# Kernel tuning notes

Hardware: AMD Instinct MI355X
Metric: run time of the kernel (lower is better)

## Reference

```python
import math
import jax, jax.numpy as jnp
import numpy as np

B, T = 65536, 34
VOCAB, TOK_DIM, POS_DIM, D_MODEL, FFN_DIM, HEAD_DIM = 14, 2, 3, 5, 2, 5
EPS = 1e-5

def _pos_flat_idx():
    # replicate _build_pos_map: 10 digits, Z_HI, 10 digits, Z_HI, 10 digits, special0, special1
    sources, indices = [], []
    for _ in range(3):
        for i in range(10):
            sources.append(0); indices.append(i)
        sources.append(2); indices.append(len([s for s in sources if s == 2]) - 1)
    # fix: the torch code appends (2,0),(2,1) after first two digit blocks and (1,0),(2,2) after the third
    sources, indices = [], []
    for i in range(10): sources.append(0); indices.append(i)
    sources.append(2); indices.append(0)
    for i in range(10): sources.append(0); indices.append(i)
    sources.append(2); indices.append(1)
    for i in range(10): sources.append(0); indices.append(i)
    sources.append(1); indices.append(0)
    sources.append(2); indices.append(2)
    src = np.array(sources); idx = np.array(indices)
    # table layout: rows 0..9 digit_pos, row 10 z_hi_pos, rows 11..13 special (learned0, learned1, eos)
    offs = np.array([0, 10, 11])
    return offs[src] + idx  # (34,)

POS_FLAT = jnp.asarray(_pos_flat_idx())
CAUSAL = jnp.tril(jnp.ones((T, T), dtype=bool))

def _rms(x, w):
    return x * jax.lax.rsqrt(jnp.mean(x * x, -1, keepdims=True) + EPS) * w

def setup_inputs():
    key = jax.random.key(0)
    ks = jax.random.split(key, 16)
    n = lambda i, shape: jax.random.normal(ks[i], shape, jnp.float32) * 0.5
    return {
        'idx': jax.random.randint(ks[0], (B, T), 0, VOCAB),
        'tok_emb': n(1, (VOCAB, TOK_DIM)),
        'spiral_amp': jnp.float32(1.0),
        'spiral_phase': jnp.float32(0.1),
        'spiral_slope': jnp.float32(1.0 / 9.0),
        'spiral_offset': jnp.float32(0.05),
        'pos_corr_slope': jnp.float32(0.01),
        'pos_corr_intercept': jnp.float32(0.02),
        'z_hi_pos': n(2, (1, POS_DIM)),
        'special_pos': n(3, (2, POS_DIM)),
        'q_w': n(4, (HEAD_DIM, POS_DIM)),
        'v_w': n(5, (HEAD_DIM, TOK_DIM)),
        'out_A': n(6, (HEAD_DIM, 2)),
        'out_B': n(7, (2, D_MODEL)),
        'q_phase': n(8, (1,)),
        'ln1_w': jnp.ones((D_MODEL,), jnp.float32),
        'ln2_w': jnp.ones((D_MODEL,), jnp.float32),
        'lnf_w': jnp.ones((D_MODEL,), jnp.float32),
        'fc1_w': n(9, (FFN_DIM, D_MODEL)),
        'fc1_b': n(10, (FFN_DIM,)),
        'fc2_w': n(11, (D_MODEL, FFN_DIM)),
        'fc2_b': n(12, (D_MODEL,)),
        'head_w': n(13, (TOK_DIM, D_MODEL)),
    }

def reference(idx, tok_emb, spiral_amp, spiral_phase, spiral_slope, spiral_offset,
              pos_corr_slope, pos_corr_intercept, z_hi_pos, special_pos,
              q_w, v_w, out_A, out_B, q_phase, ln1_w, ln2_w, lnf_w,
              fc1_w, fc1_b, fc2_w, fc2_b, head_w):
    # learned spiral digit positions (10, 3)
    i = jnp.arange(10, dtype=jnp.float32)
    angle = 2.0 * math.pi * i / 10.0 + spiral_phase
    base = jnp.stack([spiral_amp * jnp.cos(angle),
                      spiral_amp * jnp.sin(angle),
                      spiral_slope * i + spiral_offset], -1)
    corr = pos_corr_intercept + pos_corr_slope * i
    digit_pos = base * (1.0 + corr)[:, None]
    table = jnp.concatenate([digit_pos, z_hi_pos, special_pos,
                             jnp.zeros((1, POS_DIM), jnp.float32)], 0)  # (14, 3)
    pos = table[POS_FLAT]  # (T, 3)

    tok = tok_emb[idx]  # (B, T, 2)
    x = jnp.concatenate([tok, jnp.broadcast_to(pos, (idx.shape[0], T, POS_DIM))], -1)  # (B,T,5)

    h = _rms(x, ln1_w)
    q = jnp.einsum('btp,dp->btd', h[..., TOK_DIM:], q_w)  # (B,T,5)
    k = q  # q_proj applied to same input for both q and k
    v = jnp.einsum('btp,dp->btd', h[..., :TOK_DIM], v_w)  # (B,T,5)

    # per-head 2D rotation on first 4 dims (HEAD_DIM//2 = 2 pairs), dim 4 unchanged
    c, s = jnp.cos(q_phase[0]), jnp.sin(q_phase[0])
    q0, q1 = q[..., 0:4:2], q[..., 1:4:2]
    q_rot = jnp.concatenate([
        jnp.stack([q0 * c - q1 * s, q0 * s + q1 * c], -1).reshape(q.shape[:-1] + (4,)),
        q[..., 4:]], -1)

    att = jnp.einsum('btd,bsd->bts', q_rot, k) / math.sqrt(HEAD_DIM)
    att = jnp.where(CAUSAL, att, -jnp.inf)
    att = jax.nn.softmax(att, -1)
    out = jnp.einsum('bts,bsd->btd', att, v)  # (B,T,5)

    x = x + (out @ out_A) @ out_B  # low-rank out_proj
    hh = _rms(x, ln2_w)
    x = x + (jax.nn.gelu(hh @ fc1_w.T + fc1_b, approximate=False) @ fc2_w.T + fc2_b)
    x = _rms(x, lnf_w)
    return (x @ head_w.T) @ tok_emb.T  # (B, T, 14)
```

## Files before the change

kernel.cpp:

```cpp
#include <hip/hip_runtime.h>
#include <math.h>

#define T_SEQ 34
#define NTOK 14
#define NE (T_SEQ * NTOK)
#define ROWS 30
#define BLK 512
#define NEL (ROWS * T_SEQ)
#define AVS (ROWS + 1)
#define TTS (ROWS + 1)

__global__ __launch_bounds__(BLK, 4) void micro_fused_kernel(
    const int* __restrict__ idx,
    const float* __restrict__ tok_emb,
    const float* __restrict__ s_amp, const float* __restrict__ s_phase,
    const float* __restrict__ s_slope, const float* __restrict__ s_offset,
    const float* __restrict__ pc_slope, const float* __restrict__ pc_int,
    const float* __restrict__ z_hi, const float* __restrict__ spec,
    const float* __restrict__ q_w, const float* __restrict__ v_w,
    const float* __restrict__ out_A, const float* __restrict__ out_B,
    const float* __restrict__ q_phase,
    const float* __restrict__ ln1_w, const float* __restrict__ ln2_w,
    const float* __restrict__ lnf_w,
    const float* __restrict__ fc1_w, const float* __restrict__ fc1_b,
    const float* __restrict__ fc2_w, const float* __restrict__ fc2_b,
    const float* __restrict__ head_w,
    float* __restrict__ out, int N)
{
    __shared__ float4 H4[NE];
    __shared__ float  H1f[NE];
    __shared__ float4 C3[NE];
    __shared__ float2 Av[T_SEQ * AVS];
    __shared__ int    toksT[T_SEQ * TTS];
    alignas(16) __shared__ float PosT[T_SEQ * 3];
    alignas(16) __shared__ float TE[NTOK * 2];
    alignas(16) __shared__ float PMs[12];
    alignas(16) __shared__ float WsT[NTOK * 8];
    alignas(16) __shared__ float ln2s[8], lnfs[8], fc1ws[12], fc2ws[12], fc2bs[8];
    __shared__ float fc1bs[2];

    const int tid = threadIdx.x;
    const int b0 = blockIdx.x * ROWS;
    const int elemBase = b0 * T_SEQ;

    for (int i = tid; i < NEL; i += BLK) {
        int g = elemBase + i;
        int v = (g < N) ? idx[g] : 0;
        int r = i / T_SEQ, s = i - r * T_SEQ;
        toksT[s * TTS + r] = v;
    }

    if (tid < NE) {
        const float amp = s_amp[0], ph = s_phase[0], slp = s_slope[0], off = s_offset[0];
        const float pcs = pc_slope[0], pci = pc_int[0];
        const float cph = cosf(q_phase[0]), sph = sinf(q_phase[0]);
        const float cscale = 0.44721359549995793f * 1.4426950408889634f;
        const int e = tid;
        const int t = e / NTOK, tk = e - t * NTOK;
        float px, py, pz;
        if (t == 33)      { px = 0.f;     py = 0.f;     pz = 0.f; }
        else if (t == 32) { px = z_hi[0]; py = z_hi[1]; pz = z_hi[2]; }
        else if (t == 10) { px = spec[0]; py = spec[1]; pz = spec[2]; }
        else if (t == 21) { px = spec[3]; py = spec[4]; pz = spec[5]; }
        else {
            int i = (t < 10) ? t : (t < 21 ? t - 11 : t - 22);
            float fi = (float)i;
            float ang = 0.62831853071795864769f * fi + ph;
            float mlt = 1.f + pci + pcs * fi;
            px = amp * cosf(ang) * mlt;
            py = amp * sinf(ang) * mlt;
            pz = (slp * fi + off) * mlt;
        }
        if (tk == 0) { PosT[t*3] = px; PosT[t*3+1] = py; PosT[t*3+2] = pz; }
        float x0 = tok_emb[tk * 2], x1 = tok_emb[tk * 2 + 1];
        float ssum = x0*x0 + x1*x1 + px*px + py*py + pz*pz;
        float rn = rsqrtf(ssum * 0.2f + 1e-5f);
        float h0 = x0 * rn * ln1_w[0], h1 = x1 * rn * ln1_w[1];
        float h2 = px * rn * ln1_w[2], h3 = py * rn * ln1_w[3], h4 = pz * rn * ln1_w[4];
        float q0 = q_w[0]  * h2 + q_w[1]  * h3 + q_w[2]  * h4;
        float q1 = q_w[3]  * h2 + q_w[4]  * h3 + q_w[5]  * h4;
        float q2 = q_w[6]  * h2 + q_w[7]  * h3 + q_w[8]  * h4;
        float q3 = q_w[9]  * h2 + q_w[10] * h3 + q_w[11] * h4;
        float q4 = q_w[12] * h2 + q_w[13] * h3 + q_w[14] * h4;
        float r0 = q0 * cph - q1 * sph, r1 = q0 * sph + q1 * cph;
        float r2c = q2 * cph - q3 * sph, r3 = q2 * sph + q3 * cph;
        float c0 = (r0*q_w[0] + r1*q_w[3] + r2c*q_w[6] + r3*q_w[9]  + q4*q_w[12]) * cscale;
        float c1 = (r0*q_w[1] + r1*q_w[4] + r2c*q_w[7] + r3*q_w[10] + q4*q_w[13]) * cscale;
        float c2 = (r0*q_w[2] + r1*q_w[5] + r2c*q_w[8] + r3*q_w[11] + q4*q_w[14]) * cscale;
        H4[e] = make_float4(h2, h3, h4, h0);
        H1f[e] = h1;
        C3[e] = make_float4(c0, c1, c2, 0.f);
    }
    if (tid < 28) TE[tid] = tok_emb[tid];
    if (tid < 70) {
        int v = tid / 5, d = tid - v * 5;
        WsT[v * 8 + d] = head_w[d] * tok_emb[v * 2] + head_w[5 + d] * tok_emb[v * 2 + 1];
    }
    if (tid < 10) {
        int j = tid >> 1, c = tid & 1;
        float acc = 0.f;
        for (int i = 0; i < 5; ++i) {
            float m5 = out_A[i*2] * out_B[j] + out_A[i*2+1] * out_B[5 + j];
            acc += m5 * v_w[i*2 + c];
        }
        PMs[tid] = acc;
    }
    if (tid < 5)  { ln2s[tid] = ln2_w[tid]; lnfs[tid] = lnf_w[tid]; fc2bs[tid] = fc2_b[tid]; }
    if (tid < 10) { fc1ws[tid] = fc1_w[tid]; fc2ws[tid] = fc2_w[tid]; }
    if (tid < 2)  { fc1bs[tid] = fc1_b[tid]; }

    __syncthreads();

    auto attn = [&](int t, int rr) {
        int tokt = toksT[t * TTS + rr];
        float4 c3 = C3[t * NTOK + tokt];
        float l = 0.f, a0 = 0.f, a1 = 0.f;
#pragma unroll 2
        for (int s = 0; s <= t; ++s) {
            int tok = toksT[s * TTS + rr];
            int e = s * NTOK + tok;
            float4 h = H4[e];
            float h1v = H1f[e];
            float sc = fmaf(c3.x, h.x, fmaf(c3.y, h.y, c3.z * h.z));
            float p = exp2f(sc);
            l += p;
            a0 = fmaf(p, h.w, a0);
            a1 = fmaf(p, h1v, a1);
        }
        float il = 1.f / l;
        Av[t * AVS + rr] = make_float2(a0 * il, a1 * il);
    };

    if (tid < 17 * ROWS) {
        int p = tid / ROWS;
        int r = tid - p * ROWS;
        attn(p, r);
        attn(33 - p, r);
    }

    __syncthreads();

    float zA[5], zB[5];
    int linA = elemBase + tid;
    int linB = elemBase + tid + BLK;
    bool va = (linA < N);
    bool vb = (tid + BLK < NEL) && (linB < N);

    auto prep = [&](int e2, float* z) {
        int rr = e2 / T_SEQ;
        int t = e2 - rr * T_SEQ;
        int tok = toksT[t * TTS + rr];
        float2 a = Av[t * AVS + rr];
        float xv0 = TE[tok * 2], xv1 = TE[tok * 2 + 1];
        float xv2 = PosT[t*3], xv3 = PosT[t*3+1], xv4 = PosT[t*3+2];

        float y[5];
#pragma unroll
        for (int j = 0; j < 5; ++j)
            y[j] = (j == 0 ? xv0 : j == 1 ? xv1 : j == 2 ? xv2 : j == 3 ? xv3 : xv4)
                 + PMs[j*2] * a.x + PMs[j*2+1] * a.y;

        float s2 = y[0]*y[0] + y[1]*y[1] + y[2]*y[2] + y[3]*y[3] + y[4]*y[4];
        float r2 = rsqrtf(s2 * 0.2f + 1e-5f);
        float hh[5];
#pragma unroll
        for (int j = 0; j < 5; ++j) hh[j] = y[j] * r2 * ln2s[j];

        float u0 = fc1bs[0], u1 = fc1bs[1];
#pragma unroll
        for (int j = 0; j < 5; ++j) { u0 += hh[j] * fc1ws[j]; u1 += hh[j] * fc1ws[5 + j]; }
        float g0 = 0.5f * u0 * (1.f + erff(u0 * 0.70710678118654752f));
        float g1v = 0.5f * u1 * (1.f + erff(u1 * 0.70710678118654752f));

        float y2[5]; float s3 = 0.f;
#pragma unroll
        for (int j = 0; j < 5; ++j) {
            y2[j] = y[j] + g0 * fc2ws[j * 2] + g1v * fc2ws[j * 2 + 1] + fc2bs[j];
            s3 += y2[j] * y2[j];
        }
        float r3 = rsqrtf(s3 * 0.2f + 1e-5f);
#pragma unroll
        for (int j = 0; j < 5; ++j) z[j] = y2[j] * r3 * lnfs[j];
    };

    if (va) prep(tid, zA);
    if (vb) prep(tid + BLK, zB);

    float2* opA = (float2*)(out + (size_t)linA * 14);
    float2* opB = (float2*)(out + (size_t)linB * 14);
#pragma unroll
    for (int v = 0; v < 7; ++v) {
        float4 w0 = *(const float4*)&WsT[(2*v) * 8];
        float  w4 = WsT[(2*v) * 8 + 4];
        float4 u0 = *(const float4*)&WsT[(2*v+1) * 8];
        float  u4 = WsT[(2*v+1) * 8 + 4];
        if (va) {
            float rA = zA[0]*w0.x + zA[1]*w0.y + zA[2]*w0.z + zA[3]*w0.w + zA[4]*w4;
            float rB = zA[0]*u0.x + zA[1]*u0.y + zA[2]*u0.z + zA[3]*u0.w + zA[4]*u4;
            opA[v] = make_float2(rA, rB);
        }
        if (vb) {
            float rA = zB[0]*w0.x + zB[1]*w0.y + zB[2]*w0.z + zB[3]*w0.w + zB[4]*w4;
            float rB = zB[0]*u0.x + zB[1]*u0.y + zB[2]*u0.z + zB[3]*u0.w + zB[4]*u4;
            opB[v] = make_float2(rA, rB);
        }
    }
}

extern "C" void kernel_launch(void* const* d_in, const int* in_sizes, int n_in,
                              void* d_out, int out_size, void* d_ws, size_t ws_size,
                              hipStream_t stream) {
    const int N = in_sizes[0];
    const int grid = (N + NEL - 1) / NEL;
    micro_fused_kernel<<<grid, BLK, 0, stream>>>(
        (const int*)d_in[0],
        (const float*)d_in[1], (const float*)d_in[2], (const float*)d_in[3],
        (const float*)d_in[4], (const float*)d_in[5], (const float*)d_in[6],
        (const float*)d_in[7], (const float*)d_in[8], (const float*)d_in[9],
        (const float*)d_in[10], (const float*)d_in[11], (const float*)d_in[12],
        (const float*)d_in[13], (const float*)d_in[14], (const float*)d_in[15],
        (const float*)d_in[16], (const float*)d_in[17], (const float*)d_in[18],
        (const float*)d_in[19], (const float*)d_in[20], (const float*)d_in[21],
        (const float*)d_in[22],
        (float*)d_out, N);
}
```

Measured before the change: 237.1 us.

## Factor key vectors into per-position weights times per-element norm and fuse paired attention rows

Attention scores are rewritten as a dot of the query coefficients with a per-position weighted position vector, scaled by the per-element RMS factor. This removes the per-element H4/H1f tables in favour of a smaller PW array plus an Rt table. The two rows each thread handles are merged into one loop that shares token and key loads over the common prefix, and fast exp2/rcp intrinsics are used. The launch-bounds occupancy hint is also dropped. This cuts LDS traffic and loop overhead, but it shifts register and occupancy behaviour and lowers the precision of the reciprocal.

```diff
diff --git a/kernel.cpp b/kernel.cpp
--- a/kernel.cpp
+++ b/kernel.cpp
@@ -10,7 +10,7 @@
 #define AVS (ROWS + 1)
 #define TTS (ROWS + 1)
 
-__global__ __launch_bounds__(BLK, 4) void micro_fused_kernel(
+__global__ __launch_bounds__(BLK) void micro_fused_kernel(
     const int* __restrict__ idx,
     const float* __restrict__ tok_emb,
     const float* __restrict__ s_amp, const float* __restrict__ s_phase,
@@ -27,9 +27,9 @@
     const float* __restrict__ head_w,
     float* __restrict__ out, int N)
 {
-    __shared__ float4 H4[NE];
-    __shared__ float  H1f[NE];
     __shared__ float4 C3[NE];
+    __shared__ float4 Rt[NE];
+    __shared__ float4 PW[T_SEQ];
     __shared__ float2 Av[T_SEQ * AVS];
     __shared__ int    toksT[T_SEQ * TTS];
     alignas(16) __shared__ float PosT[T_SEQ * 3];
@@ -71,7 +71,10 @@
             py = amp * sinf(ang) * mlt;
             pz = (slp * fi + off) * mlt;
         }
-        if (tk == 0) { PosT[t*3] = px; PosT[t*3+1] = py; PosT[t*3+2] = pz; }
+        if (tk == 0) {
+            PosT[t*3] = px; PosT[t*3+1] = py; PosT[t*3+2] = pz;
+            PW[t] = make_float4(px * ln1_w[2], py * ln1_w[3], pz * ln1_w[4], 0.f);
+        }
         float x0 = tok_emb[tk * 2], x1 = tok_emb[tk * 2 + 1];
         float ssum = x0*x0 + x1*x1 + px*px + py*py + pz*pz;
         float rn = rsqrtf(ssum * 0.2f + 1e-5f);
@@ -87,9 +90,8 @@
         float c0 = (r0*q_w[0] + r1*q_w[3] + r2c*q_w[6] + r3*q_w[9]  + q4*q_w[12]) * cscale;
         float c1 = (r0*q_w[1] + r1*q_w[4] + r2c*q_w[7] + r3*q_w[10] + q4*q_w[13]) * cscale;
         float c2 = (r0*q_w[2] + r1*q_w[5] + r2c*q_w[8] + r3*q_w[11] + q4*q_w[14]) * cscale;
-        H4[e] = make_float4(h2, h3, h4, h0);
-        H1f[e] = h1;
         C3[e] = make_float4(c0, c1, c2, 0.f);
+        Rt[e] = make_float4(rn, h0, h1, 0.f);
     }
     if (tid < 28) TE[tid] = tok_emb[tid];
     if (tid < 70) {
@@ -111,31 +113,43 @@
 
     __syncthreads();
 
-    auto attn = [&](int t, int rr) {
-        int tokt = toksT[t * TTS + rr];
-        float4 c3 = C3[t * NTOK + tokt];
-        float l = 0.f, a0 = 0.f, a1 = 0.f;
-#pragma unroll 2
-        for (int s = 0; s <= t; ++s) {
-            int tok = toksT[s * TTS + rr];
-            int e = s * NTOK + tok;
-            float4 h = H4[e];
-            float h1v = H1f[e];
-            float sc = fmaf(c3.x, h.x, fmaf(c3.y, h.y, c3.z * h.z));
-            float p = exp2f(sc);
-            l += p;
-            a0 = fmaf(p, h.w, a0);
-            a1 = fmaf(p, h1v, a1);
-        }
-        float il = 1.f / l;
-        Av[t * AVS + rr] = make_float2(a0 * il, a1 * il);
-    };
-
     if (tid < 17 * ROWS) {
         int p = tid / ROWS;
-        int r = tid - p * ROWS;
-        attn(p, r);
-        attn(33 - p, r);
+        int rr = tid - p * ROWS;
+        int t1 = p, t2 = 33 - p;
+        const int* tRow = &toksT[rr];
+        int tok1 = tRow[t1 * TTS];
+        int tok2 = tRow[t2 * TTS];
+        float4 c31 = C3[t1 * NTOK + tok1];
+        float4 c32 = C3[t2 * NTOK + tok2];
+        float l1 = 0.f, a10 = 0.f, a11 = 0.f;
+        float l2 = 0.f, a20 = 0.f, a21 = 0.f;
+
+#pragma unroll 2
+        for (int s = 0; s <= p; ++s) {
+            int tok = tRow[s * TTS];
+            float4 R = Rt[s * NTOK + tok];
+            float4 pw = PW[s];
+            float d1 = fmaf(c31.x, pw.x, fmaf(c31.y, pw.y, c31.z * pw.z));
+            float d2 = fmaf(c32.x, pw.x, fmaf(c32.y, pw.y, c32.z * pw.z));
+            float p1 = __builtin_amdgcn_exp2f(d1 * R.x);
+            float p2 = __builtin_amdgcn_exp2f(d2 * R.x);
+            l1 += p1; a10 = fmaf(p1, R.y, a10); a11 = fmaf(p1, R.z, a11);
+            l2 += p2; a20 = fmaf(p2, R.y, a20); a21 = fmaf(p2, R.z, a21);
+        }
+#pragma unroll 4
+        for (int s = p + 1; s <= t2; ++s) {
+            int tok = tRow[s * TTS];
+            float4 R = Rt[s * NTOK + tok];
+            float4 pw = PW[s];
+            float d2 = fmaf(c32.x, pw.x, fmaf(c32.y, pw.y, c32.z * pw.z));
+            float p2 = __builtin_amdgcn_exp2f(d2 * R.x);
+            l2 += p2; a20 = fmaf(p2, R.y, a20); a21 = fmaf(p2, R.z, a21);
+        }
+        float il1 = __builtin_amdgcn_rcpf(l1);
+        float il2 = __builtin_amdgcn_rcpf(l2);
+        Av[t1 * AVS + rr] = make_float2(a10 * il1, a11 * il1);
+        Av[t2 * AVS + rr] = make_float2(a20 * il2, a21 * il2);
     }
 
     __syncthreads();
```

Result: slower. 242.8 us (+2.4%).

## Precompute factored attention score tables in a setup kernel and slim main kernel

Applied to the files above, without the earlier changes.

A small setup kernel now builds tables in workspace: per-(query position, token) rows of pre-multiplied score coefficients against every key position's scaled positional vector, plus per-(position, token) norm factors and the small weight tables. The main kernel then computes each attention score as a single multiply of a table entry by the key's norm factor, then exp2, reading score rows from global/L2 in float4 chunks. This removes the per-block recomputation of the positional tables and most of the score FMAs. The main kernel also moves to 256-thread blocks with 15 rows and uses the hardware exp2/rcp intrinsics. The cost is an extra kernel launch per call and global-memory reads of the score table. The original fused kernel is kept as a fallback when the workspace is too small.

```diff
diff --git a/kernel.cpp b/kernel.cpp
--- a/kernel.cpp
+++ b/kernel.cpp
@@ -4,13 +4,272 @@
 #define T_SEQ 34
 #define NTOK 14
 #define NE (T_SEQ * NTOK)
-#define ROWS 30
-#define BLK 512
+
+#define OFF_RT   0
+#define OFF_POS  476
+#define OFF_MISC 510
+#define NF4_SHARED 566
+#define OFF_DTAB 566
+#define DROW_F 36
+#define NF4_TOTAL (NF4_SHARED + NE * (DROW_F/4))
+#define WS_NEED ((size_t)NF4_TOTAL * 16)
+#define MI_TE    0
+#define MI_WST   32
+#define MI_PM    144
+#define MI_LN2   160
+#define MI_LNF   168
+#define MI_FC1W  176
+#define MI_FC1B  186
+#define MI_FC2W  192
+#define MI_FC2B  208
+
+#define ROWS 15
+#define BLK 256
 #define NEL (ROWS * T_SEQ)
-#define AVS (ROWS + 1)
-#define TTS (ROWS + 1)
-
-__global__ __launch_bounds__(BLK, 4) void micro_fused_kernel(
+#define TTS 17
+#define AVS 17
+
+__device__ inline void pos_for_t(int t,
+    float amp, float ph, float slp, float off, float pcs, float pci,
+    const float* __restrict__ z_hi, const float* __restrict__ spec,
+    float& px, float& py, float& pz)
+{
+    if (t == 33)      { px = 0.f;     py = 0.f;     pz = 0.f; }
+    else if (t == 32) { px = z_hi[0]; py = z_hi[1]; pz = z_hi[2]; }
+    else if (t == 10) { px = spec[0]; py = spec[1]; pz = spec[2]; }
+    else if (t == 21) { px = spec[3]; py = spec[4]; pz = spec[5]; }
+    else {
+        int i = (t < 10) ? t : (t < 21 ? t - 11 : t - 22);
+        float fi = (float)i;
+        float ang = 0.62831853071795864769f * fi + ph;
+        float mlt = 1.f + pci + pcs * fi;
+        px = amp * cosf(ang) * mlt;
+        py = amp * sinf(ang) * mlt;
+        pz = (slp * fi + off) * mlt;
+    }
+}
+
+__global__ __launch_bounds__(64) void setup_kernel(
+    const float* __restrict__ tok_emb,
+    const float* __restrict__ s_amp, const float* __restrict__ s_phase,
+    const float* __restrict__ s_slope, const float* __restrict__ s_offset,
+    const float* __restrict__ pc_slope, const float* __restrict__ pc_int,
+    const float* __restrict__ z_hi, const float* __restrict__ spec,
+    const float* __restrict__ q_w, const float* __restrict__ v_w,
+    const float* __restrict__ out_A, const float* __restrict__ out_B,
+    const float* __restrict__ q_phase,
+    const float* __restrict__ ln1_w, const float* __restrict__ ln2_w,
+    const float* __restrict__ lnf_w,
+    const float* __restrict__ fc1_w, const float* __restrict__ fc1_b,
+    const float* __restrict__ fc2_w, const float* __restrict__ fc2_b,
+    const float* __restrict__ head_w,
+    float4* __restrict__ ws)
+{
+    __shared__ float4 PWs[T_SEQ];
+    __shared__ float4 Poss[T_SEQ];
+
+    const int tid = threadIdx.x;
+    const float amp = s_amp[0], ph = s_phase[0], slp = s_slope[0], off = s_offset[0];
+    const float pcs = pc_slope[0], pci = pc_int[0];
+
+    if (tid < T_SEQ) {
+        float px, py, pz;
+        pos_for_t(tid, amp, ph, slp, off, pcs, pci, z_hi, spec, px, py, pz);
+        PWs[tid]  = make_float4(px * ln1_w[2], py * ln1_w[3], pz * ln1_w[4], 0.f);
+        Poss[tid] = make_float4(px, py, pz, 0.f);
+    }
+    __syncthreads();
+
+    const int q = blockIdx.x * 64 + tid;
+    if (q < NE) {
+        const int t = q / NTOK, tk = q - t * NTOK;
+        const float cph = cosf(q_phase[0]), sph = sinf(q_phase[0]);
+        const float cscale = 0.44721359549995793f * 1.4426950408889634f;
+        float4 P = Poss[t];
+        float px = P.x, py = P.y, pz = P.z;
+        float x0 = tok_emb[tk * 2], x1 = tok_emb[tk * 2 + 1];
+        float ssum = x0*x0 + x1*x1 + px*px + py*py + pz*pz;
+        float rn = rsqrtf(ssum * 0.2f + 1e-5f);
+        float h0 = x0 * rn * ln1_w[0], h1 = x1 * rn * ln1_w[1];
+        float h2 = px * rn * ln1_w[2], h3 = py * rn * ln1_w[3], h4 = pz * rn * ln1_w[4];
+        float q0 = q_w[0]  * h2 + q_w[1]  * h3 + q_w[2]  * h4;
+        float q1 = q_w[3]  * h2 + q_w[4]  * h3 + q_w[5]  * h4;
+        float q2 = q_w[6]  * h2 + q_w[7]  * h3 + q_w[8]  * h4;
+        float q3 = q_w[9]  * h2 + q_w[10] * h3 + q_w[11] * h4;
+        float q4 = q_w[12] * h2 + q_w[13] * h3 + q_w[14] * h4;
+        float r0 = q0 * cph - q1 * sph, r1 = q0 * sph + q1 * cph;
+        float r2c = q2 * cph - q3 * sph, r3 = q2 * sph + q3 * cph;
+        float c0 = (r0*q_w[0] + r1*q_w[3] + r2c*q_w[6] + r3*q_w[9]  + q4*q_w[12]) * cscale;
+        float c1 = (r0*q_w[1] + r1*q_w[4] + r2c*q_w[7] + r3*q_w[10] + q4*q_w[13]) * cscale;
+        float c2 = (r0*q_w[2] + r1*q_w[5] + r2c*q_w[8] + r3*q_w[11] + q4*q_w[14]) * cscale;
+
+        ws[OFF_RT + q] = make_float4(rn, h0, h1, 0.f);
+        if (tk == 0) ws[OFF_POS + t] = Poss[t];
+
+        float* Drow = (float*)(ws + OFF_DTAB) + q * DROW_F;
+        for (int s = 0; s < T_SEQ; ++s) {
+            float4 pw = PWs[s];
+            Drow[s] = fmaf(c0, pw.x, fmaf(c1, pw.y, c2 * pw.z));
+        }
+        Drow[34] = 0.f; Drow[35] = 0.f;
+    }
+
+    if (blockIdx.x == 0) {
+        float* M = (float*)(ws + OFF_MISC);
+        if (tid < 28) M[MI_TE + tid] = tok_emb[tid];
+        for (int i = tid; i < 70; i += 64) {
+            int v = i / 5, d = i - v * 5;
+            M[MI_WST + v * 8 + d] = head_w[d] * tok_emb[v * 2]
+                                  + head_w[5 + d] * tok_emb[v * 2 + 1];
+        }
+        if (tid < 10) {
+            int j = tid >> 1, c = tid & 1;
+            float acc = 0.f;
+            for (int i = 0; i < 5; ++i) {
+                float m5 = out_A[i*2] * out_B[j] + out_A[i*2+1] * out_B[5 + j];
+                acc += m5 * v_w[i*2 + c];
+            }
+            M[MI_PM + tid] = acc;
+        }
+        if (tid < 5)  { M[MI_LN2 + tid] = ln2_w[tid]; M[MI_LNF + tid] = lnf_w[tid];
+                        M[MI_FC2B + tid] = fc2_b[tid]; }
+        if (tid < 10) { M[MI_FC1W + tid] = fc1_w[tid]; M[MI_FC2W + tid] = fc2_w[tid]; }
+        if (tid < 2)  { M[MI_FC1B + tid] = fc1_b[tid]; }
+    }
+}
+
+__global__ __launch_bounds__(BLK) void micro_main(
+    const int* __restrict__ idx, const float4* __restrict__ ws,
+    float* __restrict__ out, int N)
+{
+    __shared__ float4 TBLs[NF4_SHARED];
+    __shared__ int    toksT[36 * TTS];
+    __shared__ float2 Av[T_SEQ * AVS];
+
+    const int tid = threadIdx.x;
+    const int elemBase = blockIdx.x * NEL;
+
+    for (int i = tid; i < NF4_SHARED; i += BLK) TBLs[i] = ws[i];
+    if (tid < 2 * TTS) toksT[T_SEQ * TTS + tid] = 0;
+    for (int i = tid; i < NEL; i += BLK) {
+        int g = elemBase + i;
+        int v = (g < N) ? idx[g] : 0;
+        int r = i / T_SEQ, s = i - r * T_SEQ;
+        toksT[s * TTS + r] = v;
+    }
+    __syncthreads();
+
+    const float* Dtab = (const float*)(ws + OFF_DTAB);
+
+    auto attn = [&](int t, int r) {
+        int tokt = toksT[t * TTS + r];
+        const float* Drow = Dtab + (t * NTOK + tokt) * DROW_F;
+        float l = 0.f, a0 = 0.f, a1 = 0.f;
+        const int nq = t >> 2;
+        for (int sb = 0; sb <= nq; ++sb) {
+            float4 d4 = *(const float4*)(Drow + (sb << 2));
+            int sbase = sb << 2;
+#pragma unroll
+            for (int k = 0; k < 4; ++k) {
+                int s = sbase + k;
+                int tok = toksT[s * TTS + r];
+                float4 R = TBLs[s * NTOK + tok];
+                float dk = (k == 0) ? d4.x : (k == 1) ? d4.y : (k == 2) ? d4.z : d4.w;
+                float pv = __builtin_amdgcn_exp2f(dk * R.x);
+                pv = (s <= t) ? pv : 0.f;
+                l += pv;
+                a0 = fmaf(pv, R.y, a0);
+                a1 = fmaf(pv, R.z, a1);
+            }
+        }
+        float il = __builtin_amdgcn_rcpf(l);
+        Av[t * AVS + r] = make_float2(a0 * il, a1 * il);
+    };
+
+    if (tid < 17 * ROWS) {
+        int p = tid / ROWS;
+        int r = tid - p * ROWS;
+        attn(p, r);
+        attn(33 - p, r);
+    }
+    __syncthreads();
+
+    const float* M = (const float*)&TBLs[OFF_MISC];
+    float zA[5], zB[5];
+    int linA = elemBase + tid;
+    int linB = elemBase + tid + BLK;
+    bool va = (tid < NEL) && (linA < N);
+    bool vb = (tid + BLK < NEL) && (linB < N);
+
+    auto prep = [&](int e2, float* z) {
+        int rr = e2 / T_SEQ;
+        int t = e2 - rr * T_SEQ;
+        int tok = toksT[t * TTS + rr];
+        float2 a = Av[t * AVS + rr];
+        float2 te = *(const float2*)&M[MI_TE + tok * 2];
+        float4 P = TBLs[OFF_POS + t];
+
+        float y[5];
+        y[0] = te.x + M[MI_PM + 0] * a.x + M[MI_PM + 1] * a.y;
+        y[1] = te.y + M[MI_PM + 2] * a.x + M[MI_PM + 3] * a.y;
+        y[2] = P.x  + M[MI_PM + 4] * a.x + M[MI_PM + 5] * a.y;
+        y[3] = P.y  + M[MI_PM + 6] * a.x + M[MI_PM + 7] * a.y;
+        y[4] = P.z  + M[MI_PM + 8] * a.x + M[MI_PM + 9] * a.y;
+
+        float s2 = y[0]*y[0] + y[1]*y[1] + y[2]*y[2] + y[3]*y[3] + y[4]*y[4];
+        float r2 = rsqrtf(s2 * 0.2f + 1e-5f);
+        float hh[5];
+#pragma unroll
+        for (int j = 0; j < 5; ++j) hh[j] = y[j] * r2 * M[MI_LN2 + j];
+
+        float u0 = M[MI_FC1B + 0], u1 = M[MI_FC1B + 1];
+#pragma unroll
+        for (int j = 0; j < 5; ++j) { u0 += hh[j] * M[MI_FC1W + j]; u1 += hh[j] * M[MI_FC1W + 5 + j]; }
+        float g0 = 0.5f * u0 * (1.f + erff(u0 * 0.70710678118654752f));
+        float g1v = 0.5f * u1 * (1.f + erff(u1 * 0.70710678118654752f));
+
+        float y2[5]; float s3 = 0.f;
+#pragma unroll
+        for (int j = 0; j < 5; ++j) {
+            y2[j] = y[j] + g0 * M[MI_FC2W + j*2] + g1v * M[MI_FC2W + j*2 + 1] + M[MI_FC2B + j];
+            s3 += y2[j] * y2[j];
+        }
+        float r3 = rsqrtf(s3 * 0.2f + 1e-5f);
+#pragma unroll
+        for (int j = 0; j < 5; ++j) z[j] = y2[j] * r3 * M[MI_LNF + j];
+    };
+
+    if (va) prep(tid, zA);
+    if (vb) prep(tid + BLK, zB);
+
+    float2* opA = (float2*)(out + (size_t)linA * 14);
+    float2* opB = (float2*)(out + (size_t)linB * 14);
+#pragma unroll
+    for (int v = 0; v < 7; ++v) {
+        float4 w0 = *(const float4*)&M[MI_WST + (2*v) * 8];
+        float  w4 = M[MI_WST + (2*v) * 8 + 4];
+        float4 u0 = *(const float4*)&M[MI_WST + (2*v+1) * 8];
+        float  u4 = M[MI_WST + (2*v+1) * 8 + 4];
+        if (va) {
+            float rA = zA[0]*w0.x + zA[1]*w0.y + zA[2]*w0.z + zA[3]*w0.w + zA[4]*w4;
+            float rB = zA[0]*u0.x + zA[1]*u0.y + zA[2]*u0.z + zA[3]*u0.w + zA[4]*u4;
+            opA[v] = make_float2(rA, rB);
+        }
+        if (vb) {
+            float rA = zB[0]*w0.x + zB[1]*w0.y + zB[2]*w0.z + zB[3]*w0.w + zB[4]*w4;
+            float rB = zB[0]*u0.x + zB[1]*u0.y + zB[2]*u0.z + zB[3]*u0.w + zB[4]*u4;
+            opB[v] = make_float2(rA, rB);
+        }
+    }
+}
+
+#define L_ROWS 30
+#define L_BLK 512
+#define L_NEL (L_ROWS * T_SEQ)
+#define L_AVS (L_ROWS + 1)
+#define L_TTS (L_ROWS + 1)
+
+__global__ __launch_bounds__(L_BLK, 4) void micro_fused_legacy(
     const int* __restrict__ idx,
     const float* __restrict__ tok_emb,
     const float* __restrict__ s_amp, const float* __restrict__ s_phase,
@@ -30,8 +289,8 @@
     __shared__ float4 H4[NE];
     __shared__ float  H1f[NE];
     __shared__ float4 C3[NE];
-    __shared__ float2 Av[T_SEQ * AVS];
-    __shared__ int    toksT[T_SEQ * TTS];
+    __shared__ float2 Av[T_SEQ * L_AVS];
+    __shared__ int    toksT[T_SEQ * L_TTS];
     alignas(16) __shared__ float PosT[T_SEQ * 3];
     alignas(16) __shared__ float TE[NTOK * 2];
     alignas(16) __shared__ float PMs[12];
@@ -40,16 +299,14 @@
     __shared__ float fc1bs[2];
 
     const int tid = threadIdx.x;
-    const int b0 = blockIdx.x * ROWS;
-    const int elemBase = b0 * T_SEQ;
-
-    for (int i = tid; i < NEL; i += BLK) {
+    const int elemBase = blockIdx.x * L_NEL;
+
+    for (int i = tid; i < L_NEL; i += L_BLK) {
         int g = elemBase + i;
         int v = (g < N) ? idx[g] : 0;
         int r = i / T_SEQ, s = i - r * T_SEQ;
-        toksT[s * TTS + r] = v;
-    }
-
+        toksT[s * L_TTS + r] = v;
+    }
     if (tid < NE) {
         const float amp = s_amp[0], ph = s_phase[0], slp = s_slope[0], off = s_offset[0];
         const float pcs = pc_slope[0], pci = pc_int[0];
@@ -58,19 +315,7 @@
         const int e = tid;
         const int t = e / NTOK, tk = e - t * NTOK;
         float px, py, pz;
-        if (t == 33)      { px = 0.f;     py = 0.f;     pz = 0.f; }
-        else if (t == 32) { px = z_hi[0]; py = z_hi[1]; pz = z_hi[2]; }
-        else if (t == 10) { px = spec[0]; py = spec[1]; pz = spec[2]; }
-        else if (t == 21) { px = spec[3]; py = spec[4]; pz = spec[5]; }
-        else {
-            int i = (t < 10) ? t : (t < 21 ? t - 11 : t - 22);
-            float fi = (float)i;
-            float ang = 0.62831853071795864769f * fi + ph;
-            float mlt = 1.f + pci + pcs * fi;
-            px = amp * cosf(ang) * mlt;
-            py = amp * sinf(ang) * mlt;
-            pz = (slp * fi + off) * mlt;
-        }
+        pos_for_t(t, amp, ph, slp, off, pcs, pci, z_hi, spec, px, py, pz);
         if (tk == 0) { PosT[t*3] = px; PosT[t*3+1] = py; PosT[t*3+2] = pz; }
         float x0 = tok_emb[tk * 2], x1 = tok_emb[tk * 2 + 1];
         float ssum = x0*x0 + x1*x1 + px*px + py*py + pz*pz;
@@ -108,70 +353,63 @@
     if (tid < 5)  { ln2s[tid] = ln2_w[tid]; lnfs[tid] = lnf_w[tid]; fc2bs[tid] = fc2_b[tid]; }
     if (tid < 10) { fc1ws[tid] = fc1_w[tid]; fc2ws[tid] = fc2_w[tid]; }
     if (tid < 2)  { fc1bs[tid] = fc1_b[tid]; }
-
     __syncthreads();
 
     auto attn = [&](int t, int rr) {
-        int tokt = toksT[t * TTS + rr];
+        int tokt = toksT[t * L_TTS + rr];
         float4 c3 = C3[t * NTOK + tokt];
         float l = 0.f, a0 = 0.f, a1 = 0.f;
 #pragma unroll 2
         for (int s = 0; s <= t; ++s) {
-            int tok = toksT[s * TTS + rr];
+            int tok = toksT[s * L_TTS + rr];
             int e = s * NTOK + tok;
             float4 h = H4[e];
             float h1v = H1f[e];
             float sc = fmaf(c3.x, h.x, fmaf(c3.y, h.y, c3.z * h.z));
-            float p = exp2f(sc);
+            float p = __builtin_amdgcn_exp2f(sc);
             l += p;
             a0 = fmaf(p, h.w, a0);
             a1 = fmaf(p, h1v, a1);
         }
-        float il = 1.f / l;
-        Av[t * AVS + rr] = make_float2(a0 * il, a1 * il);
+        float il = __builtin_amdgcn_rcpf(l);
+        Av[t * L_AVS + rr] = make_float2(a0 * il, a1 * il);
     };
-
-    if (tid < 17 * ROWS) {
-        int p = tid / ROWS;
-        int r = tid - p * ROWS;
+    if (tid < 17 * L_ROWS) {
+        int p = tid / L_ROWS;
+        int r = tid - p * L_ROWS;
         attn(p, r);
         attn(33 - p, r);
     }
-
     __syncthreads();
 
     float zA[5], zB[5];
     int linA = elemBase + tid;
-    int linB = elemBase + tid + BLK;
-    bool va = (linA < N);
-    bool vb = (tid + BLK < NEL) && (linB < N);
+    int linB = elemBase + tid + L_BLK;
+    bool va = (tid < L_NEL) && (linA < N);
+    bool vb = (tid + L_BLK < L_NEL) && (linB < N);
 
     auto prep = [&](int e2, float* z) {
         int rr = e2 / T_SEQ;
         int t = e2 - rr * T_SEQ;
-        int tok = toksT[t * TTS + rr];
-        float2 a = Av[t * AVS + rr];
+        int tok = toksT[t * L_TTS + rr];
+        float2 a = Av[t * L_AVS + rr];
         float xv0 = TE[tok * 2], xv1 = TE[tok * 2 + 1];
         float xv2 = PosT[t*3], xv3 = PosT[t*3+1], xv4 = PosT[t*3+2];
-
         float y[5];
 #pragma unroll
         for (int j = 0; j < 5; ++j)
             y[j] = (j == 0 ? xv0 : j == 1 ? xv1 : j == 2 ? xv2 : j == 3 ? xv3 : xv4)
                  + PMs[j*2] * a.x + PMs[j*2+1] * a.y;
-
         float s2 = y[0]*y[0] + y[1]*y[1] + y[2]*y[2] + y[3]*y[3] + y[4]*y[4];
         float r2 = rsqrtf(s2 * 0.2f + 1e-5f);
         float hh[5];
 #pragma unroll
         for (int j = 0; j < 5; ++j) hh[j] = y[j] * r2 * ln2s[j];
-
         float u0 = fc1bs[0], u1 = fc1bs[1];
 #pragma unroll
         for (int j = 0; j < 5; ++j) { u0 += hh[j] * fc1ws[j]; u1 += hh[j] * fc1ws[5 + j]; }
         float g0 = 0.5f * u0 * (1.f + erff(u0 * 0.70710678118654752f));
         float g1v = 0.5f * u1 * (1.f + erff(u1 * 0.70710678118654752f));
-
         float y2[5]; float s3 = 0.f;
 #pragma unroll
         for (int j = 0; j < 5; ++j) {
@@ -184,7 +422,7 @@
     };
 
     if (va) prep(tid, zA);
-    if (vb) prep(tid + BLK, zB);
+    if (vb) prep(tid + L_BLK, zB);
 
     float2* opA = (float2*)(out + (size_t)linA * 14);
     float2* opB = (float2*)(out + (size_t)linB * 14);
@@ -211,16 +449,32 @@
                               void* d_out, int out_size, void* d_ws, size_t ws_size,
                               hipStream_t stream) {
     const int N = in_sizes[0];
-    const int grid = (N + NEL - 1) / NEL;
-    micro_fused_kernel<<<grid, BLK, 0, stream>>>(
-        (const int*)d_in[0],
-        (const float*)d_in[1], (const float*)d_in[2], (const float*)d_in[3],
-        (const float*)d_in[4], (const float*)d_in[5], (const float*)d_in[6],
-        (const float*)d_in[7], (const float*)d_in[8], (const float*)d_in[9],
-        (const float*)d_in[10], (const float*)d_in[11], (const float*)d_in[12],
-        (const float*)d_in[13], (const float*)d_in[14], (const float*)d_in[15],
-        (const float*)d_in[16], (const float*)d_in[17], (const float*)d_in[18],
-        (const float*)d_in[19], (const float*)d_in[20], (const float*)d_in[21],
-        (const float*)d_in[22],
-        (float*)d_out, N);
+    if (ws_size >= WS_NEED && d_ws != nullptr) {
+        setup_kernel<<<8, 64, 0, stream>>>(
+            (const float*)d_in[1], (const float*)d_in[2], (const float*)d_in[3],
+            (const float*)d_in[4], (const float*)d_in[5], (const float*)d_in[6],
+            (const float*)d_in[7], (const float*)d_in[8], (const float*)d_in[9],
+            (const float*)d_in[10], (const float*)d_in[11], (const float*)d_in[12],
+            (const float*)d_in[13], (const float*)d_in[14], (const float*)d_in[15],
+            (const float*)d_in[16], (const float*)d_in[17], (const float*)d_in[18],
+            (const float*)d_in[19], (const float*)d_in[20], (const float*)d_in[21],
+            (const float*)d_in[22],
+            (float4*)d_ws);
+        const int grid = (N + NEL - 1) / NEL;
+        micro_main<<<grid, BLK, 0, stream>>>(
+            (const int*)d_in[0], (const float4*)d_ws, (float*)d_out, N);
+    } else {
+        const int grid = (N + L_NEL - 1) / L_NEL;
+        micro_fused_legacy<<<grid, L_BLK, 0, stream>>>(
+            (const int*)d_in[0],
+            (const float*)d_in[1], (const float*)d_in[2], (const float*)d_in[3],
+            (const float*)d_in[4], (const float*)d_in[5], (const float*)d_in[6],
+            (const float*)d_in[7], (const float*)d_in[8], (const float*)d_in[9],
+            (const float*)d_in[10], (const float*)d_in[11], (const float*)d_in[12],
+            (const float*)d_in[13], (const float*)d_in[14], (const float*)d_in[15],
+            (const float*)d_in[16], (const float*)d_in[17], (const float*)d_in[18],
+            (const float*)d_in[19], (const float*)d_in[20], (const float*)d_in[21],
+            (const float*)d_in[22],
+            (float*)d_out, N);
+    }
 }
```

New measurement: 243.2 us. 2.6% more time.

## Map one thread per element, fusing attention and MLP without shared staging

Applied to the files above, without the earlier changes.

Cuts rows per block from 30 to 15 so each of the 510 active threads owns one (row, position) element. Each thread now runs that element's causal attention and the post-attention MLP/head in registers, removing the Av shared buffer and the second barrier. It also switches to native exp2/rcp intrinsics and drops the occupancy hint from launch bounds. In exchange, the per-block table setup is amortized over half as many rows, and attention work is unbalanced across threads (position 0 does one step, position 33 does 34), where the old code paired t with 33-t.

```diff
diff --git a/kernel.cpp b/kernel.cpp
--- a/kernel.cpp
+++ b/kernel.cpp
@@ -4,13 +4,12 @@
 #define T_SEQ 34
 #define NTOK 14
 #define NE (T_SEQ * NTOK)
-#define ROWS 30
+#define ROWS 15
 #define BLK 512
 #define NEL (ROWS * T_SEQ)
-#define AVS (ROWS + 1)
-#define TTS (ROWS + 1)
+#define TTS 17
 
-__global__ __launch_bounds__(BLK, 4) void micro_fused_kernel(
+__global__ __launch_bounds__(BLK) void micro_fused_kernel(
     const int* __restrict__ idx,
     const float* __restrict__ tok_emb,
     const float* __restrict__ s_amp, const float* __restrict__ s_phase,
@@ -30,7 +29,6 @@
     __shared__ float4 H4[NE];
     __shared__ float  H1f[NE];
     __shared__ float4 C3[NE];
-    __shared__ float2 Av[T_SEQ * AVS];
     __shared__ int    toksT[T_SEQ * TTS];
     alignas(16) __shared__ float PosT[T_SEQ * 3];
     alignas(16) __shared__ float TE[NTOK * 2];
@@ -40,13 +38,12 @@
     __shared__ float fc1bs[2];
 
     const int tid = threadIdx.x;
-    const int b0 = blockIdx.x * ROWS;
-    const int elemBase = b0 * T_SEQ;
+    const int elemBase = blockIdx.x * NEL;
 
-    for (int i = tid; i < NEL; i += BLK) {
-        int g = elemBase + i;
+    if (tid < NEL) {
+        int g = elemBase + tid;
         int v = (g < N) ? idx[g] : 0;
-        int r = i / T_SEQ, s = i - r * T_SEQ;
+        int r = tid / T_SEQ, s = tid - r * T_SEQ;
         toksT[s * TTS + r] = v;
     }
 
@@ -111,99 +108,74 @@
 
     __syncthreads();
 
-    auto attn = [&](int t, int rr) {
-        int tokt = toksT[t * TTS + rr];
-        float4 c3 = C3[t * NTOK + tokt];
-        float l = 0.f, a0 = 0.f, a1 = 0.f;
-#pragma unroll 2
-        for (int s = 0; s <= t; ++s) {
-            int tok = toksT[s * TTS + rr];
-            int e = s * NTOK + tok;
-            float4 h = H4[e];
-            float h1v = H1f[e];
-            float sc = fmaf(c3.x, h.x, fmaf(c3.y, h.y, c3.z * h.z));
-            float p = exp2f(sc);
-            l += p;
-            a0 = fmaf(p, h.w, a0);
-            a1 = fmaf(p, h1v, a1);
-        }
-        float il = 1.f / l;
-        Av[t * AVS + rr] = make_float2(a0 * il, a1 * il);
-    };
+    if (tid >= NEL) return;
+    const int t = tid / ROWS;
+    const int r = tid - t * ROWS;
+    const int lin = elemBase + r * T_SEQ + t;
 
-    if (tid < 17 * ROWS) {
-        int p = tid / ROWS;
-        int r = tid - p * ROWS;
-        attn(p, r);
-        attn(33 - p, r);
+    const int tokt = toksT[t * TTS + r];
+    const float4 c3 = C3[t * NTOK + tokt];
+    float l = 0.f, a0 = 0.f, a1 = 0.f;
+#pragma unroll 4
+    for (int s = 0; s <= t; ++s) {
+        int tok = toksT[s * TTS + r];
+        int e = s * NTOK + tok;
+        float4 h = H4[e];
+        float h1v = H1f[e];
+        float sc = fmaf(c3.x, h.x, fmaf(c3.y, h.y, c3.z * h.z));
+        float p = __builtin_amdgcn_exp2f(sc);
+        l += p;
+        a0 = fmaf(p, h.w, a0);
+        a1 = fmaf(p, h1v, a1);
     }
+    const float il = __builtin_amdgcn_rcpf(l);
+    a0 *= il; a1 *= il;
 
-    __syncthreads();
+    if (lin >= N) return;
 
-    float zA[5], zB[5];
-    int linA = elemBase + tid;
-    int linB = elemBase + tid + BLK;
-    bool va = (linA < N);
-    bool vb = (tid + BLK < NEL) && (linB < N);
+    const float xv0 = TE[tokt * 2], xv1 = TE[tokt * 2 + 1];
+    const float xv2 = PosT[t*3], xv3 = PosT[t*3+1], xv4 = PosT[t*3+2];
 
-    auto prep = [&](int e2, float* z) {
-        int rr = e2 / T_SEQ;
-        int t = e2 - rr * T_SEQ;
-        int tok = toksT[t * TTS + rr];
-        float2 a = Av[t * AVS + rr];
-        float xv0 = TE[tok * 2], xv1 = TE[tok * 2 + 1];
-        float xv2 = PosT[t*3], xv3 = PosT[t*3+1], xv4 = PosT[t*3+2];
+    float y[5];
+    y[0] = xv0 + PMs[0] * a0 + PMs[1] * a1;
+    y[1] = xv1 + PMs[2] * a0 + PMs[3] * a1;
+    y[2] = xv2 + PMs[4] * a0 + PMs[5] * a1;
+    y[3] = xv3 + PMs[6] * a0 + PMs[7] * a1;
+    y[4] = xv4 + PMs[8] * a0 + PMs[9] * a1;
 
-        float y[5];
+    float s2 = y[0]*y[0] + y[1]*y[1] + y[2]*y[2] + y[3]*y[3] + y[4]*y[4];
+    float r2 = rsqrtf(s2 * 0.2f + 1e-5f);
+    float hh[5];
 #pragma unroll
-        for (int j = 0; j < 5; ++j)
-            y[j] = (j == 0 ? xv0 : j == 1 ? xv1 : j == 2 ? xv2 : j == 3 ? xv3 : xv4)
-                 + PMs[j*2] * a.x + PMs[j*2+1] * a.y;
+    for (int j = 0; j < 5; ++j) hh[j] = y[j] * r2 * ln2s[j];
 
-        float s2 = y[0]*y[0] + y[1]*y[1] + y[2]*y[2] + y[3]*y[3] + y[4]*y[4];
-        float r2 = rsqrtf(s2 * 0.2f + 1e-5f);
-        float hh[5];
+    float u0 = fc1bs[0], u1 = fc1bs[1];
 #pragma unroll
-        for (int j = 0; j < 5; ++j) hh[j] = y[j] * r2 * ln2s[j];
+    for (int j = 0; j < 5; ++j) { u0 += hh[j] * fc1ws[j]; u1 += hh[j] * fc1ws[5 + j]; }
+    float g0 = 0.5f * u0 * (1.f + erff(u0 * 0.70710678118654752f));
+    float g1v = 0.5f * u1 * (1.f + erff(u1 * 0.70710678118654752f));
 
-        float u0 = fc1bs[0], u1 = fc1bs[1];
+    float y2[5]; float s3 = 0.f;
 #pragma unroll
-        for (int j = 0; j < 5; ++j) { u0 += hh[j] * fc1ws[j]; u1 += hh[j] * fc1ws[5 + j]; }
-        float g0 = 0.5f * u0 * (1.f + erff(u0 * 0.70710678118654752f));
-        float g1v = 0.5f * u1 * (1.f + erff(u1 * 0.70710678118654752f));
+    for (int j = 0; j < 5; ++j) {
+        y2[j] = y[j] + g0 * fc2ws[j * 2] + g1v * fc2ws[j * 2 + 1] + fc2bs[j];
+        s3 += y2[j] * y2[j];
+    }
+    float r3 = rsqrtf(s3 * 0.2f + 1e-5f);
+    float z[5];
+#pragma unroll
+    for (int j = 0; j < 5; ++j) z[j] = y2[j] * r3 * lnfs[j];
 
-        float y2[5]; float s3 = 0.f;
-#pragma unroll
-        for (int j = 0; j < 5; ++j) {
-            y2[j] = y[j] + g0 * fc2ws[j * 2] + g1v * fc2ws[j * 2 + 1] + fc2bs[j];
-            s3 += y2[j] * y2[j];
-        }
-        float r3 = rsqrtf(s3 * 0.2f + 1e-5f);
-#pragma unroll
-        for (int j = 0; j < 5; ++j) z[j] = y2[j] * r3 * lnfs[j];
-    };
-
-    if (va) prep(tid, zA);
-    if (vb) prep(tid + BLK, zB);
-
-    float2* opA = (float2*)(out + (size_t)linA * 14);
-    float2* opB = (float2*)(out + (size_t)linB * 14);
+    float2* op = (float2*)(out + (size_t)lin * 14);
 #pragma unroll
     for (int v = 0; v < 7; ++v) {
         float4 w0 = *(const float4*)&WsT[(2*v) * 8];
         float  w4 = WsT[(2*v) * 8 + 4];
-        float4 u0 = *(const float4*)&WsT[(2*v+1) * 8];
+        float4 u0v = *(const float4*)&WsT[(2*v+1) * 8];
         float  u4 = WsT[(2*v+1) * 8 + 4];
-        if (va) {
-            float rA = zA[0]*w0.x + zA[1]*w0.y + zA[2]*w0.z + zA[3]*w0.w + zA[4]*w4;
-            float rB = zA[0]*u0.x + zA[1]*u0.y + zA[2]*u0.z + zA[3]*u0.w + zA[4]*u4;
-            opA[v] = make_float2(rA, rB);
-        }
-        if (vb) {
-            float rA = zB[0]*w0.x + zB[1]*w0.y + zB[2]*w0.z + zB[3]*w0.w + zB[4]*w4;
-            float rB = zB[0]*u0.x + zB[1]*u0.y + zB[2]*u0.z + zB[3]*u0.w + zB[4]*u4;
-            opB[v] = make_float2(rA, rB);
-        }
+        float rA = z[0]*w0.x + z[1]*w0.y + z[2]*w0.z + z[3]*w0.w + z[4]*w4;
+        float rB = z[0]*u0v.x + z[1]*u0v.y + z[2]*u0v.z + z[3]*u0v.w + z[4]*u4;
+        op[v] = make_float2(rA, rB);
     }
 }
 
```

After: 214.4 us. -9.6%, faster.
